# Performance work log

Hardware: AMD Instinct MI355X
Metric: run time of the kernel (lower is better)

Reference implementation:

```python
import jax, jax.numpy as jnp
import numpy as np

SIZE = 768
INNER = 64

def setup_inputs() -> dict:
    key = jax.random.key(0)
    ks = jax.random.split(key, 7)
    emb_input = jax.random.normal(ks[0], (8, 2048, SIZE), dtype=jnp.float32)
    s = 1.0 / np.sqrt(SIZE)
    Wq = jax.random.normal(ks[1], (INNER, SIZE), dtype=jnp.float32) * s
    bq = jax.random.normal(ks[2], (INNER,), dtype=jnp.float32) * 0.01
    Wk = jax.random.normal(ks[3], (INNER, SIZE), dtype=jnp.float32) * s
    bk = jax.random.normal(ks[4], (INNER,), dtype=jnp.float32) * 0.01
    Wv = jax.random.normal(ks[5], (INNER, SIZE), dtype=jnp.float32) * s
    bv = jax.random.normal(ks[6], (INNER,), dtype=jnp.float32) * 0.01
    return {"emb_input": emb_input, "Wq": Wq, "bq": bq, "Wk": Wk, "bk": bk, "Wv": Wv, "bv": bv}

def reference(emb_input, Wq, bq, Wk, bk, Wv, bv):
    # q,k,v: (B,S,inner)
    q = jnp.einsum('bse,ie->bsi', emb_input, Wq) + bq
    k = jnp.einsum('bse,ie->bsi', emb_input, Wk) + bk
    v = jnp.einsum('bse,ie->bsi', emb_input, Wv) + bv
    # NOTE: original scales by sqrt(emb_size), not sqrt(inner_size)
    scale = 1.0 / np.sqrt(SIZE).astype(np.float32)
    attn = jnp.einsum('bqi,bki->bqk', q, k) * scale  # (B,S,S)
    attn = jax.nn.softmax(attn, axis=2)
    # attn @ v, same math as original broadcast-mul-sum but as a matmul
    return jnp.einsum('bqk,bki->bqi', attn, v)
```

## Files before the change

### kernel.cpp

```cpp
#include <hip/hip_runtime.h>
#include <hip/hip_bf16.h>
#include <math.h>

#define B_  8
#define S_  2048
#define E_  768
#define I_  64

typedef __attribute__((ext_vector_type(4))) float f32x4;
typedef __attribute__((ext_vector_type(8))) short short8;
typedef __attribute__((ext_vector_type(4))) short short4v;

static __device__ __forceinline__ short bf16_of(float x) {
    unsigned u = __builtin_bit_cast(unsigned, x);
    u += 0x7fffu + ((u >> 16) & 1u);
    return (short)(u >> 16);
}

static __device__ __forceinline__ unsigned pk2(float lo, float hi) {
    __hip_bfloat162 h = __float22bfloat162_rn(float2{lo, hi});
    unsigned u; __builtin_memcpy(&u, &h, 4);
    return u;
}
static __device__ __forceinline__ short8 pk8(f32x4 a, f32x4 b) {
    union { unsigned u[4]; short8 s; } r;
    r.u[0] = pk2(a[0], a[1]); r.u[1] = pk2(a[2], a[3]);
    r.u[2] = pk2(b[0], b[1]); r.u[3] = pk2(b[2], b[3]);
    return r.s;
}

typedef __attribute__((address_space(1))) const void gv_t;
typedef __attribute__((address_space(3))) void lv_t;
static __device__ __forceinline__ void gload16(const void* g, void* l) {
    __builtin_amdgcn_global_load_lds((gv_t*)g, (lv_t*)l, 16, 0, 0);
}

#define BARRIER()   asm volatile("s_barrier" ::: "memory")
#define VMCNT(n)    asm volatile("s_waitcnt vmcnt(" #n ")" ::: "memory")

__global__ void wconv(const float* __restrict__ Wq, const float* __restrict__ bq,
                      const float* __restrict__ Wk, const float* __restrict__ bk,
                      const float* __restrict__ Wv, const float* __restrict__ bv,
                      short* __restrict__ Wb, float* __restrict__ bb, float qscale) {
    int r = blockIdx.x;
    const float* src; const float* bsrc; float sc;
    if (r < 64)       { src = Wq + r * E_;         bsrc = bq + r;         sc = qscale; }
    else if (r < 128) { src = Wk + (r - 64) * E_;  bsrc = bk + (r - 64);  sc = 1.0f; }
    else              { src = Wv + (r - 128) * E_; bsrc = bv + (r - 128); sc = 1.0f; }
    for (int j = threadIdx.x; j < E_; j += blockDim.x)
        Wb[r * E_ + j] = bf16_of(src[j] * sc);
    if (threadIdx.x == 0) bb[r] = bsrc[0] * sc;
}

__global__ __launch_bounds__(256) void qkv_proj(
    const float* __restrict__ emb, const short* __restrict__ Wb,
    const float* __restrict__ bb,
    short* __restrict__ qb, short* __restrict__ kb, short* __restrict__ vT)
{
    __shared__ float Af[2][32][64];
    __shared__ short Wf[2][192][64];

    const int tid = threadIdx.x, w = tid >> 6, l = tid & 63;
    const int lr = l & 15, rg = l >> 4;
    const int sm = w & 1, sc = w >> 1;
    const int m0 = blockIdx.x * 32;

    f32x4 acc[6];
#pragma unroll
    for (int t = 0; t < 6; ++t) acc[t] = (f32x4){0.f, 0.f, 0.f, 0.f};

    auto STAGE = [&](int ks, int d) {
        char* ab = (char*)&Af[d][0][0] + w * 2048;
#pragma unroll
        for (int i = 0; i < 2; ++i) {
            int r = w * 8 + i * 4 + (l >> 4);
            const float* src = emb + (size_t)(m0 + r) * E_ + ks * 64 + (((l & 15) ^ (r & 15)) << 2);
            gload16(src, ab + i * 1024);
        }
        char* wb2 = (char*)&Wf[d][0][0] + w * 6144;
#pragma unroll
        for (int i = 0; i < 6; ++i) {
            int r = w * 48 + i * 8 + (l >> 3);
            const short* src = Wb + (size_t)r * E_ + ks * 64 + (((l & 7) ^ (r & 7)) << 3);
            gload16(src, wb2 + i * 1024);
        }
    };

    STAGE(0, 0);
    STAGE(1, 1);

    for (int ks = 0; ks < 12; ++ks) {
        const int cur = ks & 1;
        if (ks == 11) { VMCNT(0); } else { VMCNT(8); }
        BARRIER();
#pragma unroll
        for (int h = 0; h < 2; ++h) {
            const int r = sm * 16 + lr;
            const int s0 = (h * 8 + rg * 2) ^ lr;
            const int s1 = (h * 8 + rg * 2 + 1) ^ lr;
            f32x4 a0 = *(const f32x4*)&Af[cur][r][s0 * 4];
            f32x4 a1 = *(const f32x4*)&Af[cur][r][s1 * 4];
            short8 af = pk8(a0, a1);
#pragma unroll
            for (int tt = 0; tt < 6; ++tt) {
                int rw = (sc * 6 + tt) * 16 + lr;
                short8 wf = *(const short8*)&Wf[cur][rw][((h * 4 + rg) ^ (lr & 7)) << 3];
                acc[tt] = __builtin_amdgcn_mfma_f32_16x16x32_bf16(af, wf, acc[tt], 0, 0, 0);
            }
        }
        BARRIER();
        if (ks + 2 < 12) STAGE(ks + 2, cur);
    }

#pragma unroll
    for (int tt = 0; tt < 6; ++tt) {
        int col = sc * 96 + tt * 16 + lr;
        float bias = bb[col];
        int row = m0 + sm * 16 + rg * 4;
        if (col < 64) {
#pragma unroll
            for (int j = 0; j < 4; ++j)
                qb[(size_t)(row + j) * 64 + col] = bf16_of(acc[tt][j] + bias);
        } else if (col < 128) {
#pragma unroll
            for (int j = 0; j < 4; ++j)
                kb[(size_t)(row + j) * 64 + (col - 64)] = bf16_of(acc[tt][j] + bias);
        } else {
            short4v pv;
#pragma unroll
            for (int j = 0; j < 4; ++j) pv[j] = bf16_of(acc[tt][j] + bias);
            int b = row >> 11, s = row & 2047;
            *(short4v*)&vT[((size_t)b * 64 + (col - 128)) * S_ + s] = pv;
        }
    }
}

__global__ __launch_bounds__(512) void flash_attn(
    const short* __restrict__ qb, const short* __restrict__ kb,
    const short* __restrict__ vT, float* __restrict__ out)
{
    __shared__ __align__(16) char smem[81920];
    short (*Kb)[2][64][64] = (short(*)[2][64][64])(smem);
    short (*Vb)[2][64][64] = (short(*)[2][64][64])(smem + 32768);
    uint2 (*pbuf)[16][16]  = (uint2(*)[16][16]) (smem + 65536);
    float (*mbuf)[64][16]  = (float(*)[64][16])(smem);
    float (*rsb)[16]       = (float(*)[16])    (smem + 16384);

    const int tid = threadIdx.x, w = tid >> 6, l = tid & 63;
    const int lr = l & 15, rg = l >> 4;
    const int g = w & 3, c = w >> 2;
    const int batch = blockIdx.x & 7;
    const int qt = blockIdx.x >> 3;
    const int qloc0 = qt * 64 + g * 16;

    const short* kbB = kb + (size_t)batch * S_ * 64;
    const short* vTB = vT + (size_t)batch * 64 * S_;

    const int swsrc = ((l & 7) ^ (l >> 3)) << 3;
    auto STAGE = [&](int ks, int d) {
        const int kt = c * 16 + ks;
        const int rl = g * 16 + (l >> 3);
        char* kd = (char*)&Kb[c][d][0][0] + g * 2048;
        gload16(kbB + (size_t)(kt * 64 + rl) * 64 + swsrc, kd);
        gload16(kbB + (size_t)(kt * 64 + rl + 8) * 64 + swsrc, kd + 1024);
        char* vd = (char*)&Vb[c][d][0][0] + g * 2048;
        gload16(vTB + (size_t)rl * S_ + kt * 64 + swsrc, vd);
        gload16(vTB + (size_t)(rl + 8) * S_ + kt * 64 + swsrc, vd + 1024);
    };

    short8 aq0 = *(const short8*)(qb + (size_t)(batch * S_ + qloc0 + lr) * 64 + rg * 8);
    short8 aq1 = *(const short8*)(qb + (size_t)(batch * S_ + qloc0 + lr) * 64 + 32 + rg * 8);

    f32x4 acc[4];
    float rs = 0.f;
#pragma unroll
    for (int n = 0; n < 4; ++n) acc[n] = (f32x4){0.f, 0.f, 0.f, 0.f};

    const int Mu = (lr & 7) << 1;
    uint2* pwr[4];
#pragma unroll
    for (int t = 0; t < 4; ++t) pwr[t] = &pbuf[w][lr][(t * 4 + rg) ^ Mu];
    const uint2* prd0 = &pbuf[w][lr][(rg * 2) ^ Mu];
    const uint2* prd1 = &pbuf[w][lr][(8 + rg * 2) ^ Mu];

    STAGE(0, 0);
    STAGE(1, 1);

    for (int ks = 0; ks < 16; ++ks) {
        const int cur = ks & 1;
        if (ks == 15) { VMCNT(0); } else { VMCNT(4); }
        BARRIER();

        f32x4 s2[4];
#pragma unroll
        for (int t = 0; t < 4; ++t) {
            const int rk = t * 16 + lr;
            short8 kf0 = *(const short8*)&Kb[c][cur][rk][((0 * 4 + rg) ^ (lr & 7)) << 3];
            short8 kf1 = *(const short8*)&Kb[c][cur][rk][((1 * 4 + rg) ^ (lr & 7)) << 3];
            f32x4 z = (f32x4){0.f, 0.f, 0.f, 0.f};
            z = __builtin_amdgcn_mfma_f32_16x16x32_bf16(kf0, aq0, z, 0, 0, 0);
            s2[t] = __builtin_amdgcn_mfma_f32_16x16x32_bf16(kf1, aq1, z, 0, 0, 0);
        }
#pragma unroll
        for (int t = 0; t < 4; ++t) {
            float p0 = __builtin_amdgcn_exp2f(s2[t][0]);
            float p1 = __builtin_amdgcn_exp2f(s2[t][1]);
            float p2 = __builtin_amdgcn_exp2f(s2[t][2]);
            float p3 = __builtin_amdgcn_exp2f(s2[t][3]);
            rs += (p0 + p1) + (p2 + p3);
            *pwr[t] = uint2{pk2(p0, p1), pk2(p2, p3)};
        }
        short8 pa0 = *(const short8*)prd0;
        short8 pa1 = *(const short8*)prd1;
#pragma unroll
        for (int n = 0; n < 4; ++n) {
            const int ri = n * 16 + lr;
            short8 v0 = *(const short8*)&Vb[c][cur][ri][((0 * 4 + rg) ^ (lr & 7)) << 3];
            short8 v1 = *(const short8*)&Vb[c][cur][ri][((1 * 4 + rg) ^ (lr & 7)) << 3];
            acc[n] = __builtin_amdgcn_mfma_f32_16x16x32_bf16(pa0, v0, acc[n], 0, 0, 0);
            acc[n] = __builtin_amdgcn_mfma_f32_16x16x32_bf16(pa1, v1, acc[n], 0, 0, 0);
        }

        BARRIER();
        if (ks + 2 < 16) STAGE(ks + 2, cur);
    }

    rs += __shfl_xor(rs, 16, 64);
    rs += __shfl_xor(rs, 32, 64);

    if (c == 1) {
#pragma unroll
        for (int n = 0; n < 4; ++n)
#pragma unroll
            for (int j = 0; j < 4; ++j) mbuf[g][l][n * 4 + j] = acc[n][j];
        if (l < 16) rsb[g][l] = rs;
    }
    __syncthreads();
    if (c == 0) {
        const int qrow = batch * S_ + qloc0 + rg * 4;
#pragma unroll
        for (int j = 0; j < 4; ++j) {
            const int qj = rg * 4 + j;
            float inv = 1.0f / (__shfl(rs, qj, 64) + rsb[g][qj]);
            float* orow = out + (size_t)(qrow + j) * 64;
#pragma unroll
            for (int n = 0; n < 4; ++n)
                orow[n * 16 + lr] = (acc[n][j] + mbuf[g][l][n * 4 + j]) * inv;
        }
    }
}

extern "C" void kernel_launch(void* const* d_in, const int* in_sizes, int n_in,
                              void* d_out, int out_size, void* d_ws, size_t ws_size,
                              hipStream_t stream) {
    const float* emb = (const float*)d_in[0];
    const float* Wq  = (const float*)d_in[1];
    const float* bq  = (const float*)d_in[2];
    const float* Wk  = (const float*)d_in[3];
    const float* bk  = (const float*)d_in[4];
    const float* Wv  = (const float*)d_in[5];
    const float* bv  = (const float*)d_in[6];
    float* out = (float*)d_out;

    char* ws = (char*)d_ws;
    short* Wb  = (short*)(ws + 0);
    float* bb  = (float*)(ws + 294912);
    short* qb  = (short*)(ws + 295680);
    short* kb  = (short*)(ws + 295680 + 2097152);
    short* vT  = (short*)(ws + 295680 + 2 * 2097152);

    const float qscale = 1.4426950408889634f / sqrtf((float)E_);

    hipLaunchKernelGGL(wconv, dim3(192), dim3(256), 0, stream,
                       Wq, bq, Wk, bk, Wv, bv, Wb, bb, qscale);
    hipLaunchKernelGGL(qkv_proj, dim3(512), dim3(256), 0, stream,
                       emb, Wb, bb, qb, kb, vT);
    hipLaunchKernelGGL(flash_attn, dim3(256), dim3(512), 0, stream,
                       qb, kb, vT, out);
}
```

Measured before the change: 41.26 us.

## Fuse weight conversion, QKV projection and attention into one cooperative kernel

Merges the three kernels into a single cooperative launch of 256 blocks of 512 threads, with grid-wide syncs between weight conversion, QKV projection and flash attention. The projection is retiled to 64 rows per block with 8 waves so the grid matches the attention launch. This removes two kernel-launch gaps and their tail effects, at the cost of grid.sync overhead and a projection phase that now uses half as many blocks with more work each, which may lower latency hiding.

```diff
diff --git a/kernel.cpp b/kernel.cpp
--- a/kernel.cpp
+++ b/kernel.cpp
@@ -1,6 +1,9 @@
 #include <hip/hip_runtime.h>
 #include <hip/hip_bf16.h>
+#include <hip/hip_cooperative_groups.h>
 #include <math.h>
+
+namespace cg = cooperative_groups;
 
 #define B_  8
 #define S_  2048
@@ -38,214 +41,229 @@
 #define BARRIER()   asm volatile("s_barrier" ::: "memory")
 #define VMCNT(n)    asm volatile("s_waitcnt vmcnt(" #n ")" ::: "memory")
 
-__global__ void wconv(const float* __restrict__ Wq, const float* __restrict__ bq,
-                      const float* __restrict__ Wk, const float* __restrict__ bk,
-                      const float* __restrict__ Wv, const float* __restrict__ bv,
-                      short* __restrict__ Wb, float* __restrict__ bb, float qscale) {
-    int r = blockIdx.x;
-    const float* src; const float* bsrc; float sc;
-    if (r < 64)       { src = Wq + r * E_;         bsrc = bq + r;         sc = qscale; }
-    else if (r < 128) { src = Wk + (r - 64) * E_;  bsrc = bk + (r - 64);  sc = 1.0f; }
-    else              { src = Wv + (r - 128) * E_; bsrc = bv + (r - 128); sc = 1.0f; }
-    for (int j = threadIdx.x; j < E_; j += blockDim.x)
-        Wb[r * E_ + j] = bf16_of(src[j] * sc);
-    if (threadIdx.x == 0) bb[r] = bsrc[0] * sc;
-}
-
-__global__ __launch_bounds__(256) void qkv_proj(
-    const float* __restrict__ emb, const short* __restrict__ Wb,
-    const float* __restrict__ bb,
-    short* __restrict__ qb, short* __restrict__ kb, short* __restrict__ vT)
+__global__ __launch_bounds__(512) void fused_attn(
+    const float* __restrict__ emb,
+    const float* __restrict__ Wq, const float* __restrict__ bq,
+    const float* __restrict__ Wk, const float* __restrict__ bk,
+    const float* __restrict__ Wv, const float* __restrict__ bv,
+    short* __restrict__ Wb, float* __restrict__ bb,
+    short* __restrict__ qb, short* __restrict__ kb, short* __restrict__ vT,
+    float* __restrict__ out, float qscale)
 {
-    __shared__ float Af[2][32][64];
-    __shared__ short Wf[2][192][64];
+    __shared__ __align__(16) char smem[81920];
+    cg::grid_group grid = cg::this_grid();
 
     const int tid = threadIdx.x, w = tid >> 6, l = tid & 63;
     const int lr = l & 15, rg = l >> 4;
-    const int sm = w & 1, sc = w >> 1;
-    const int m0 = blockIdx.x * 32;
-
-    f32x4 acc[6];
-#pragma unroll
-    for (int t = 0; t < 6; ++t) acc[t] = (f32x4){0.f, 0.f, 0.f, 0.f};
-
-    auto STAGE = [&](int ks, int d) {
-        char* ab = (char*)&Af[d][0][0] + w * 2048;
-#pragma unroll
-        for (int i = 0; i < 2; ++i) {
-            int r = w * 8 + i * 4 + (l >> 4);
-            const float* src = emb + (size_t)(m0 + r) * E_ + ks * 64 + (((l & 15) ^ (r & 15)) << 2);
-            gload16(src, ab + i * 1024);
-        }
-        char* wb2 = (char*)&Wf[d][0][0] + w * 6144;
-#pragma unroll
-        for (int i = 0; i < 6; ++i) {
-            int r = w * 48 + i * 8 + (l >> 3);
-            const short* src = Wb + (size_t)r * E_ + ks * 64 + (((l & 7) ^ (r & 7)) << 3);
-            gload16(src, wb2 + i * 1024);
-        }
-    };
-
-    STAGE(0, 0);
-    STAGE(1, 1);
-
-    for (int ks = 0; ks < 12; ++ks) {
-        const int cur = ks & 1;
-        if (ks == 11) { VMCNT(0); } else { VMCNT(8); }
-        BARRIER();
-#pragma unroll
-        for (int h = 0; h < 2; ++h) {
-            const int r = sm * 16 + lr;
-            const int s0 = (h * 8 + rg * 2) ^ lr;
-            const int s1 = (h * 8 + rg * 2 + 1) ^ lr;
-            f32x4 a0 = *(const f32x4*)&Af[cur][r][s0 * 4];
-            f32x4 a1 = *(const f32x4*)&Af[cur][r][s1 * 4];
-            short8 af = pk8(a0, a1);
-#pragma unroll
-            for (int tt = 0; tt < 6; ++tt) {
-                int rw = (sc * 6 + tt) * 16 + lr;
-                short8 wf = *(const short8*)&Wf[cur][rw][((h * 4 + rg) ^ (lr & 7)) << 3];
-                acc[tt] = __builtin_amdgcn_mfma_f32_16x16x32_bf16(af, wf, acc[tt], 0, 0, 0);
-            }
-        }
-        BARRIER();
-        if (ks + 2 < 12) STAGE(ks + 2, cur);
+    const int bid = blockIdx.x;
+
+    {
+        const int gid = bid * 512 + tid;
+#pragma unroll
+        for (int ii = 0; ii < 2; ++ii) {
+            int i = gid + ii * 131072;
+            if (i < 192 * 768) {
+                int r = i / 768, j = i - r * 768;
+                const float* src; float sc;
+                if (r < 64)       { src = Wq + r * 768;         sc = qscale; }
+                else if (r < 128) { src = Wk + (r - 64) * 768;  sc = 1.0f; }
+                else              { src = Wv + (r - 128) * 768; sc = 1.0f; }
+                Wb[i] = bf16_of(src[j] * sc);
+            }
+        }
+        if (gid < 192) {
+            const float* bsrc; float sc;
+            if (gid < 64)       { bsrc = bq + gid;       sc = qscale; }
+            else if (gid < 128) { bsrc = bk + gid - 64;  sc = 1.0f; }
+            else                { bsrc = bv + gid - 128; sc = 1.0f; }
+            bb[gid] = bsrc[0] * sc;
+        }
     }
-
-#pragma unroll
-    for (int tt = 0; tt < 6; ++tt) {
-        int col = sc * 96 + tt * 16 + lr;
-        float bias = bb[col];
-        int row = m0 + sm * 16 + rg * 4;
-        if (col < 64) {
-#pragma unroll
-            for (int j = 0; j < 4; ++j)
-                qb[(size_t)(row + j) * 64 + col] = bf16_of(acc[tt][j] + bias);
-        } else if (col < 128) {
-#pragma unroll
-            for (int j = 0; j < 4; ++j)
-                kb[(size_t)(row + j) * 64 + (col - 64)] = bf16_of(acc[tt][j] + bias);
-        } else {
-            short4v pv;
-#pragma unroll
-            for (int j = 0; j < 4; ++j) pv[j] = bf16_of(acc[tt][j] + bias);
-            int b = row >> 11, s = row & 2047;
-            *(short4v*)&vT[((size_t)b * 64 + (col - 128)) * S_ + s] = pv;
+    grid.sync();
+
+    {
+        float (*Af)[64][64]  = (float(*)[64][64]) (smem);
+        short (*Wf)[192][64] = (short(*)[192][64])(smem + 32768);
+        const int sm = w & 3, scc = w >> 2;
+        const int m0 = bid * 64;
+
+        f32x4 acc[6];
+#pragma unroll
+        for (int t = 0; t < 6; ++t) acc[t] = (f32x4){0.f, 0.f, 0.f, 0.f};
+
+        auto STAGE = [&](int ks, int d) {
+            char* ab = (char*)&Af[d][0][0] + w * 2048;
+#pragma unroll
+            for (int i = 0; i < 2; ++i) {
+                int r = w * 8 + i * 4 + (l >> 4);
+                const float* src = emb + (size_t)(m0 + r) * E_ + ks * 64 + (((l & 15) ^ (r & 15)) << 2);
+                gload16(src, ab + i * 1024);
+            }
+            char* wb2 = (char*)&Wf[d][0][0] + w * 3072;
+#pragma unroll
+            for (int i = 0; i < 3; ++i) {
+                int r = w * 24 + i * 8 + (l >> 3);
+                const short* src = Wb + (size_t)r * E_ + ks * 64 + (((l & 7) ^ (r & 7)) << 3);
+                gload16(src, wb2 + i * 1024);
+            }
+        };
+
+        STAGE(0, 0);
+        STAGE(1, 1);
+
+        for (int ks = 0; ks < 12; ++ks) {
+            const int cur = ks & 1;
+            if (ks == 11) { VMCNT(0); } else { VMCNT(5); }
+            BARRIER();
+#pragma unroll
+            for (int h = 0; h < 2; ++h) {
+                const int r = sm * 16 + lr;
+                const int s0 = (h * 8 + rg * 2) ^ lr;
+                const int s1 = (h * 8 + rg * 2 + 1) ^ lr;
+                f32x4 a0 = *(const f32x4*)&Af[cur][r][s0 * 4];
+                f32x4 a1 = *(const f32x4*)&Af[cur][r][s1 * 4];
+                short8 af = pk8(a0, a1);
+#pragma unroll
+                for (int tt = 0; tt < 6; ++tt) {
+                    int rw = (scc * 6 + tt) * 16 + lr;
+                    short8 wf = *(const short8*)&Wf[cur][rw][((h * 4 + rg) ^ (lr & 7)) << 3];
+                    acc[tt] = __builtin_amdgcn_mfma_f32_16x16x32_bf16(af, wf, acc[tt], 0, 0, 0);
+                }
+            }
+            BARRIER();
+            if (ks + 2 < 12) STAGE(ks + 2, cur);
+        }
+
+#pragma unroll
+        for (int tt = 0; tt < 6; ++tt) {
+            int col = scc * 96 + tt * 16 + lr;
+            float bias = bb[col];
+            int row = m0 + sm * 16 + rg * 4;
+            if (col < 64) {
+#pragma unroll
+                for (int j = 0; j < 4; ++j)
+                    qb[(size_t)(row + j) * 64 + col] = bf16_of(acc[tt][j] + bias);
+            } else if (col < 128) {
+#pragma unroll
+                for (int j = 0; j < 4; ++j)
+                    kb[(size_t)(row + j) * 64 + (col - 64)] = bf16_of(acc[tt][j] + bias);
+            } else {
+                short4v pv;
+#pragma unroll
+                for (int j = 0; j < 4; ++j) pv[j] = bf16_of(acc[tt][j] + bias);
+                int b = row >> 11, s = row & 2047;
+                *(short4v*)&vT[((size_t)b * 64 + (col - 128)) * S_ + s] = pv;
+            }
         }
     }
-}
-
-__global__ __launch_bounds__(512) void flash_attn(
-    const short* __restrict__ qb, const short* __restrict__ kb,
-    const short* __restrict__ vT, float* __restrict__ out)
-{
-    __shared__ __align__(16) char smem[81920];
-    short (*Kb)[2][64][64] = (short(*)[2][64][64])(smem);
-    short (*Vb)[2][64][64] = (short(*)[2][64][64])(smem + 32768);
-    uint2 (*pbuf)[16][16]  = (uint2(*)[16][16]) (smem + 65536);
-    float (*mbuf)[64][16]  = (float(*)[64][16])(smem);
-    float (*rsb)[16]       = (float(*)[16])    (smem + 16384);
-
-    const int tid = threadIdx.x, w = tid >> 6, l = tid & 63;
-    const int lr = l & 15, rg = l >> 4;
-    const int g = w & 3, c = w >> 2;
-    const int batch = blockIdx.x & 7;
-    const int qt = blockIdx.x >> 3;
-    const int qloc0 = qt * 64 + g * 16;
-
-    const short* kbB = kb + (size_t)batch * S_ * 64;
-    const short* vTB = vT + (size_t)batch * 64 * S_;
-
-    const int swsrc = ((l & 7) ^ (l >> 3)) << 3;
-    auto STAGE = [&](int ks, int d) {
-        const int kt = c * 16 + ks;
-        const int rl = g * 16 + (l >> 3);
-        char* kd = (char*)&Kb[c][d][0][0] + g * 2048;
-        gload16(kbB + (size_t)(kt * 64 + rl) * 64 + swsrc, kd);
-        gload16(kbB + (size_t)(kt * 64 + rl + 8) * 64 + swsrc, kd + 1024);
-        char* vd = (char*)&Vb[c][d][0][0] + g * 2048;
-        gload16(vTB + (size_t)rl * S_ + kt * 64 + swsrc, vd);
-        gload16(vTB + (size_t)(rl + 8) * S_ + kt * 64 + swsrc, vd + 1024);
-    };
-
-    short8 aq0 = *(const short8*)(qb + (size_t)(batch * S_ + qloc0 + lr) * 64 + rg * 8);
-    short8 aq1 = *(const short8*)(qb + (size_t)(batch * S_ + qloc0 + lr) * 64 + 32 + rg * 8);
-
-    f32x4 acc[4];
-    float rs = 0.f;
-#pragma unroll
-    for (int n = 0; n < 4; ++n) acc[n] = (f32x4){0.f, 0.f, 0.f, 0.f};
-
-    const int Mu = (lr & 7) << 1;
-    uint2* pwr[4];
-#pragma unroll
-    for (int t = 0; t < 4; ++t) pwr[t] = &pbuf[w][lr][(t * 4 + rg) ^ Mu];
-    const uint2* prd0 = &pbuf[w][lr][(rg * 2) ^ Mu];
-    const uint2* prd1 = &pbuf[w][lr][(8 + rg * 2) ^ Mu];
-
-    STAGE(0, 0);
-    STAGE(1, 1);
-
-    for (int ks = 0; ks < 16; ++ks) {
-        const int cur = ks & 1;
-        if (ks == 15) { VMCNT(0); } else { VMCNT(4); }
-        BARRIER();
-
-        f32x4 s2[4];
-#pragma unroll
-        for (int t = 0; t < 4; ++t) {
-            const int rk = t * 16 + lr;
-            short8 kf0 = *(const short8*)&Kb[c][cur][rk][((0 * 4 + rg) ^ (lr & 7)) << 3];
-            short8 kf1 = *(const short8*)&Kb[c][cur][rk][((1 * 4 + rg) ^ (lr & 7)) << 3];
-            f32x4 z = (f32x4){0.f, 0.f, 0.f, 0.f};
-            z = __builtin_amdgcn_mfma_f32_16x16x32_bf16(kf0, aq0, z, 0, 0, 0);
-            s2[t] = __builtin_amdgcn_mfma_f32_16x16x32_bf16(kf1, aq1, z, 0, 0, 0);
-        }
-#pragma unroll
-        for (int t = 0; t < 4; ++t) {
-            float p0 = __builtin_amdgcn_exp2f(s2[t][0]);
-            float p1 = __builtin_amdgcn_exp2f(s2[t][1]);
-            float p2 = __builtin_amdgcn_exp2f(s2[t][2]);
-            float p3 = __builtin_amdgcn_exp2f(s2[t][3]);
-            rs += (p0 + p1) + (p2 + p3);
-            *pwr[t] = uint2{pk2(p0, p1), pk2(p2, p3)};
-        }
-        short8 pa0 = *(const short8*)prd0;
-        short8 pa1 = *(const short8*)prd1;
-#pragma unroll
-        for (int n = 0; n < 4; ++n) {
-            const int ri = n * 16 + lr;
-            short8 v0 = *(const short8*)&Vb[c][cur][ri][((0 * 4 + rg) ^ (lr & 7)) << 3];
-            short8 v1 = *(const short8*)&Vb[c][cur][ri][((1 * 4 + rg) ^ (lr & 7)) << 3];
-            acc[n] = __builtin_amdgcn_mfma_f32_16x16x32_bf16(pa0, v0, acc[n], 0, 0, 0);
-            acc[n] = __builtin_amdgcn_mfma_f32_16x16x32_bf16(pa1, v1, acc[n], 0, 0, 0);
-        }
-
-        BARRIER();
-        if (ks + 2 < 16) STAGE(ks + 2, cur);
-    }
-
-    rs += __shfl_xor(rs, 16, 64);
-    rs += __shfl_xor(rs, 32, 64);
-
-    if (c == 1) {
-#pragma unroll
-        for (int n = 0; n < 4; ++n)
-#pragma unroll
-            for (int j = 0; j < 4; ++j) mbuf[g][l][n * 4 + j] = acc[n][j];
-        if (l < 16) rsb[g][l] = rs;
-    }
-    __syncthreads();
-    if (c == 0) {
-        const int qrow = batch * S_ + qloc0 + rg * 4;
-#pragma unroll
-        for (int j = 0; j < 4; ++j) {
-            const int qj = rg * 4 + j;
-            float inv = 1.0f / (__shfl(rs, qj, 64) + rsb[g][qj]);
-            float* orow = out + (size_t)(qrow + j) * 64;
+    grid.sync();
+
+    {
+        short (*Kb)[2][64][64] = (short(*)[2][64][64])(smem);
+        short (*Vb)[2][64][64] = (short(*)[2][64][64])(smem + 32768);
+        uint2 (*pbuf)[16][16]  = (uint2(*)[16][16]) (smem + 65536);
+        float (*mbuf)[64][16]  = (float(*)[64][16])(smem);
+        float (*rsb)[16]       = (float(*)[16])    (smem + 16384);
+
+        const int g = w & 3, c = w >> 2;
+        const int batch = bid & 7;
+        const int qt = bid >> 3;
+        const int qloc0 = qt * 64 + g * 16;
+
+        const short* kbB = kb + (size_t)batch * S_ * 64;
+        const short* vTB = vT + (size_t)batch * 64 * S_;
+
+        const int swsrc = ((l & 7) ^ (l >> 3)) << 3;
+        auto STAGE = [&](int ks, int d) {
+            const int kt = c * 16 + ks;
+            const int rl = g * 16 + (l >> 3);
+            char* kd = (char*)&Kb[c][d][0][0] + g * 2048;
+            gload16(kbB + (size_t)(kt * 64 + rl) * 64 + swsrc, kd);
+            gload16(kbB + (size_t)(kt * 64 + rl + 8) * 64 + swsrc, kd + 1024);
+            char* vd = (char*)&Vb[c][d][0][0] + g * 2048;
+            gload16(vTB + (size_t)rl * S_ + kt * 64 + swsrc, vd);
+            gload16(vTB + (size_t)(rl + 8) * S_ + kt * 64 + swsrc, vd + 1024);
+        };
+
+        short8 aq0 = *(const short8*)(qb + (size_t)(batch * S_ + qloc0 + lr) * 64 + rg * 8);
+        short8 aq1 = *(const short8*)(qb + (size_t)(batch * S_ + qloc0 + lr) * 64 + 32 + rg * 8);
+
+        f32x4 acc[4];
+        float rs = 0.f;
+#pragma unroll
+        for (int n = 0; n < 4; ++n) acc[n] = (f32x4){0.f, 0.f, 0.f, 0.f};
+
+        const int Mu = (lr & 7) << 1;
+        uint2* pwr[4];
+#pragma unroll
+        for (int t = 0; t < 4; ++t) pwr[t] = &pbuf[w][lr][(t * 4 + rg) ^ Mu];
+        const uint2* prd0 = &pbuf[w][lr][(rg * 2) ^ Mu];
+        const uint2* prd1 = &pbuf[w][lr][(8 + rg * 2) ^ Mu];
+
+        STAGE(0, 0);
+        STAGE(1, 1);
+
+        for (int ks = 0; ks < 16; ++ks) {
+            const int cur = ks & 1;
+            if (ks == 15) { VMCNT(0); } else { VMCNT(4); }
+            BARRIER();
+
+            f32x4 s2[4];
+#pragma unroll
+            for (int t = 0; t < 4; ++t) {
+                const int rk = t * 16 + lr;
+                short8 kf0 = *(const short8*)&Kb[c][cur][rk][((0 * 4 + rg) ^ (lr & 7)) << 3];
+                short8 kf1 = *(const short8*)&Kb[c][cur][rk][((1 * 4 + rg) ^ (lr & 7)) << 3];
+                f32x4 z = (f32x4){0.f, 0.f, 0.f, 0.f};
+                z = __builtin_amdgcn_mfma_f32_16x16x32_bf16(kf0, aq0, z, 0, 0, 0);
+                s2[t] = __builtin_amdgcn_mfma_f32_16x16x32_bf16(kf1, aq1, z, 0, 0, 0);
+            }
+#pragma unroll
+            for (int t = 0; t < 4; ++t) {
+                float p0 = __builtin_amdgcn_exp2f(s2[t][0]);
+                float p1 = __builtin_amdgcn_exp2f(s2[t][1]);
+                float p2 = __builtin_amdgcn_exp2f(s2[t][2]);
+                float p3 = __builtin_amdgcn_exp2f(s2[t][3]);
+                rs += (p0 + p1) + (p2 + p3);
+                *pwr[t] = uint2{pk2(p0, p1), pk2(p2, p3)};
+            }
+            short8 pa0 = *(const short8*)prd0;
+            short8 pa1 = *(const short8*)prd1;
+#pragma unroll
+            for (int n = 0; n < 4; ++n) {
+                const int ri = n * 16 + lr;
+                short8 v0 = *(const short8*)&Vb[c][cur][ri][((0 * 4 + rg) ^ (lr & 7)) << 3];
+                short8 v1 = *(const short8*)&Vb[c][cur][ri][((1 * 4 + rg) ^ (lr & 7)) << 3];
+                acc[n] = __builtin_amdgcn_mfma_f32_16x16x32_bf16(pa0, v0, acc[n], 0, 0, 0);
+                acc[n] = __builtin_amdgcn_mfma_f32_16x16x32_bf16(pa1, v1, acc[n], 0, 0, 0);
+            }
+
+            BARRIER();
+            if (ks + 2 < 16) STAGE(ks + 2, cur);
+        }
+
+        rs += __shfl_xor(rs, 16, 64);
+        rs += __shfl_xor(rs, 32, 64);
+
+        if (c == 1) {
 #pragma unroll
             for (int n = 0; n < 4; ++n)
-                orow[n * 16 + lr] = (acc[n][j] + mbuf[g][l][n * 4 + j]) * inv;
+#pragma unroll
+                for (int j = 0; j < 4; ++j) mbuf[g][l][n * 4 + j] = acc[n][j];
+            if (l < 16) rsb[g][l] = rs;
+        }
+        __syncthreads();
+        if (c == 0) {
+            const int qrow = batch * S_ + qloc0 + rg * 4;
+#pragma unroll
+            for (int j = 0; j < 4; ++j) {
+                const int qj = rg * 4 + j;
+                float inv = 1.0f / (__shfl(rs, qj, 64) + rsb[g][qj]);
+                float* orow = out + (size_t)(qrow + j) * 64;
+#pragma unroll
+                for (int n = 0; n < 4; ++n)
+                    orow[n * 16 + lr] = (acc[n][j] + mbuf[g][l][n * 4 + j]) * inv;
+            }
         }
     }
 }
@@ -269,12 +287,11 @@
     short* kb  = (short*)(ws + 295680 + 2097152);
     short* vT  = (short*)(ws + 295680 + 2 * 2097152);
 
-    const float qscale = 1.4426950408889634f / sqrtf((float)E_);
-
-    hipLaunchKernelGGL(wconv, dim3(192), dim3(256), 0, stream,
-                       Wq, bq, Wk, bk, Wv, bv, Wb, bb, qscale);
-    hipLaunchKernelGGL(qkv_proj, dim3(512), dim3(256), 0, stream,
-                       emb, Wb, bb, qb, kb, vT);
-    hipLaunchKernelGGL(flash_attn, dim3(256), dim3(512), 0, stream,
-                       qb, kb, vT, out);
-}
+    float qscale = 1.4426950408889634f / sqrtf((float)E_);
+
+    void* args[] = {(void*)&emb, (void*)&Wq, (void*)&bq, (void*)&Wk, (void*)&bk,
+                    (void*)&Wv, (void*)&bv, (void*)&Wb, (void*)&bb,
+                    (void*)&qb, (void*)&kb, (void*)&vT, (void*)&out, (void*)&qscale};
+    (void)hipLaunchCooperativeKernel((const void*)fused_attn, dim3(256), dim3(512),
+                                     args, 0, stream);
+}
```

New measurement: 94.83 us. +129.8%, slower.

## Split attention keys four ways per block and read V fragments from global

Applied to the files above, without the earlier changes.

The attention kernel now processes 32 queries per block, with four wave pairs each covering a quarter of the key sequence. This doubles the grid to 512 blocks. V is no longer staged through LDS; each wave loads its V fragments straight from global memory into registers, and only K is double-buffered in shared memory. The final merge sums partial accumulators and row sums from three peer key-chunks through LDS, and launch bounds now request higher occupancy. This aims for more parallelism and less LDS traffic, at the cost of uncoalesced global V reads, more cross-wave reduction work, and K tiles reloaded by twice as many blocks.

```diff
diff --git a/kernel.cpp b/kernel.cpp
--- a/kernel.cpp
+++ b/kernel.cpp
@@ -135,37 +135,32 @@
     }
 }
 
-__global__ __launch_bounds__(512) void flash_attn(
+__global__ __launch_bounds__(512, 4) void flash_attn(
     const short* __restrict__ qb, const short* __restrict__ kb,
     const short* __restrict__ vT, float* __restrict__ out)
 {
     __shared__ __align__(16) char smem[81920];
     short (*Kb)[2][64][64] = (short(*)[2][64][64])(smem);
-    short (*Vb)[2][64][64] = (short(*)[2][64][64])(smem + 32768);
-    uint2 (*pbuf)[16][16]  = (uint2(*)[16][16]) (smem + 65536);
-    float (*mbuf)[64][16]  = (float(*)[64][16])(smem);
-    float (*rsb)[16]       = (float(*)[16])    (smem + 16384);
+    uint2 (*pbuf)[16][16]  = (uint2(*)[16][16])(smem + 65536);
 
     const int tid = threadIdx.x, w = tid >> 6, l = tid & 63;
     const int lr = l & 15, rg = l >> 4;
-    const int g = w & 3, c = w >> 2;
+    const int c = w >> 1, g = w & 1;
     const int batch = blockIdx.x & 7;
     const int qt = blockIdx.x >> 3;
-    const int qloc0 = qt * 64 + g * 16;
+    const int qloc0 = qt * 32 + g * 16;
 
     const short* kbB = kb + (size_t)batch * S_ * 64;
     const short* vTB = vT + (size_t)batch * 64 * S_;
 
-    const int swsrc = ((l & 7) ^ (l >> 3)) << 3;
-    auto STAGE = [&](int ks, int d) {
-        const int kt = c * 16 + ks;
-        const int rl = g * 16 + (l >> 3);
-        char* kd = (char*)&Kb[c][d][0][0] + g * 2048;
-        gload16(kbB + (size_t)(kt * 64 + rl) * 64 + swsrc, kd);
-        gload16(kbB + (size_t)(kt * 64 + rl + 8) * 64 + swsrc, kd + 1024);
-        char* vd = (char*)&Vb[c][d][0][0] + g * 2048;
-        gload16(vTB + (size_t)rl * S_ + kt * 64 + swsrc, vd);
-        gload16(vTB + (size_t)(rl + 8) * S_ + kt * 64 + swsrc, vd + 1024);
+    const int swk = ((l & 7) ^ (l >> 3)) << 3;
+    auto STAGE = [&](int ks2, int d) {
+        const int k0 = c * 512 + ks2 * 64;
+        char* kd = (char*)&Kb[c][d][0][0] + g * 4096;
+#pragma unroll
+        for (int i = 0; i < 4; ++i)
+            gload16(kbB + (size_t)(k0 + g * 32 + i * 8 + (l >> 3)) * 64 + swk,
+                    kd + i * 1024);
     };
 
     short8 aq0 = *(const short8*)(qb + (size_t)(batch * S_ + qloc0 + lr) * 64 + rg * 8);
@@ -186,10 +181,18 @@
     STAGE(0, 0);
     STAGE(1, 1);
 
-    for (int ks = 0; ks < 16; ++ks) {
+    for (int ks = 0; ks < 8; ++ks) {
         const int cur = ks & 1;
-        if (ks == 15) { VMCNT(0); } else { VMCNT(4); }
-        BARRIER();
+        if (ks == 7) { VMCNT(0); } else { VMCNT(4); }
+        BARRIER();
+
+        const int k0 = c * 512 + ks * 64;
+        short8 vf[2][4];
+#pragma unroll
+        for (int h = 0; h < 2; ++h)
+#pragma unroll
+            for (int n = 0; n < 4; ++n)
+                vf[h][n] = *(const short8*)(vTB + (size_t)(n * 16 + lr) * S_ + k0 + h * 32 + rg * 8);
 
         f32x4 s2[4];
 #pragma unroll
@@ -214,26 +217,26 @@
         short8 pa1 = *(const short8*)prd1;
 #pragma unroll
         for (int n = 0; n < 4; ++n) {
-            const int ri = n * 16 + lr;
-            short8 v0 = *(const short8*)&Vb[c][cur][ri][((0 * 4 + rg) ^ (lr & 7)) << 3];
-            short8 v1 = *(const short8*)&Vb[c][cur][ri][((1 * 4 + rg) ^ (lr & 7)) << 3];
-            acc[n] = __builtin_amdgcn_mfma_f32_16x16x32_bf16(pa0, v0, acc[n], 0, 0, 0);
-            acc[n] = __builtin_amdgcn_mfma_f32_16x16x32_bf16(pa1, v1, acc[n], 0, 0, 0);
-        }
-
-        BARRIER();
-        if (ks + 2 < 16) STAGE(ks + 2, cur);
+            acc[n] = __builtin_amdgcn_mfma_f32_16x16x32_bf16(pa0, vf[0][n], acc[n], 0, 0, 0);
+            acc[n] = __builtin_amdgcn_mfma_f32_16x16x32_bf16(pa1, vf[1][n], acc[n], 0, 0, 0);
+        }
+
+        BARRIER();
+        if (ks + 2 < 8) STAGE(ks + 2, cur);
     }
 
     rs += __shfl_xor(rs, 16, 64);
     rs += __shfl_xor(rs, 32, 64);
 
-    if (c == 1) {
+    if (c != 0) {
+        float* mp = (float*)(smem + w * 4096);
+        float* rp = (float*)(smem + 32768 + w * 256);
 #pragma unroll
         for (int n = 0; n < 4; ++n)
 #pragma unroll
-            for (int j = 0; j < 4; ++j) mbuf[g][l][n * 4 + j] = acc[n][j];
-        if (l < 16) rsb[g][l] = rs;
+            for (int j = 0; j < 4; ++j)
+                mp[l * 16 + n * 4 + j] = acc[n][j];
+        if (l < 16) rp[l] = rs;
     }
     __syncthreads();
     if (c == 0) {
@@ -241,11 +244,20 @@
 #pragma unroll
         for (int j = 0; j < 4; ++j) {
             const int qj = rg * 4 + j;
-            float inv = 1.0f / (__shfl(rs, qj, 64) + rsb[g][qj]);
+            float tot = __shfl(rs, qj, 64);
+#pragma unroll
+            for (int cc = 1; cc < 4; ++cc)
+                tot += ((const float*)(smem + 32768 + (cc * 2 + g) * 256))[qj];
+            float inv = 1.0f / tot;
             float* orow = out + (size_t)(qrow + j) * 64;
 #pragma unroll
-            for (int n = 0; n < 4; ++n)
-                orow[n * 16 + lr] = (acc[n][j] + mbuf[g][l][n * 4 + j]) * inv;
+            for (int n = 0; n < 4; ++n) {
+                float v = acc[n][j];
+#pragma unroll
+                for (int cc = 1; cc < 4; ++cc)
+                    v += ((const float*)(smem + (cc * 2 + g) * 4096))[l * 16 + n * 4 + j];
+                orow[n * 16 + lr] = v * inv;
+            }
         }
     }
 }
@@ -275,6 +287,6 @@
                        Wq, bq, Wk, bk, Wv, bv, Wb, bb, qscale);
     hipLaunchKernelGGL(qkv_proj, dim3(512), dim3(256), 0, stream,
                        emb, Wb, bb, qb, kb, vT);
-    hipLaunchKernelGGL(flash_attn, dim3(256), dim3(512), 0, stream,
+    hipLaunchKernelGGL(flash_attn, dim3(512), dim3(512), 0, stream,
                        qb, kb, vT, out);
 }
```

Result: slower. 60.71 us (+47.1%).
